# Optimization experiments

Hardware: AMD Instinct MI355X
Metric: run time of the kernel (lower is better)

The kernel has to match this reference:

```python
import jax, jax.numpy as jnp
import numpy as np

B, S, D, H = 64, 2048, 512, 512


def setup_inputs() -> dict:
    key = jax.random.key(0)
    ks = jax.random.split(key, 8)
    inp = jax.random.normal(ks[0], (B, D), dtype=jnp.float32)
    context = jax.random.normal(ks[1], (B, S, D), dtype=jnp.float32)
    mask = jax.random.randint(ks[2], (B, S), 0, 2).astype(jnp.int32)
    alpha_mask = jax.random.uniform(ks[3], (B, S), dtype=jnp.float32)
    sd = 1.0 / np.sqrt(D)
    W_in = jax.random.uniform(ks[4], (H, D), minval=-sd, maxval=sd, dtype=jnp.float32)
    b_in = jnp.zeros((H,), dtype=jnp.float32)
    W_ctx = jax.random.uniform(ks[5], (H, D), minval=-sd, maxval=sd, dtype=jnp.float32)  # Conv1d k=1 == pointwise linear
    b_ctx = jnp.zeros((H,), dtype=jnp.float32)
    V = jax.random.uniform(ks[6], (H,), minval=-1.0, maxval=1.0, dtype=jnp.float32)
    return {"input": inp, "context": context, "alpha_mask": alpha_mask,
            "W_in": W_in, "b_in": b_in, "W_ctx": W_ctx, "b_ctx": b_ctx, "V": V,
            "mask": mask}


def reference(input, context, alpha_mask, W_in, b_in, W_ctx, b_ctx, V, mask):
    seq_len = context.shape[1]
    # input_linear: [B, H]
    inp = input @ W_in.T + b_in
    # context_linear (Conv1d kernel=1 over permuted context): [B, H, S]
    ctx = jnp.einsum('hd,bsd->bhs', W_ctx, context) + b_ctx[None, :, None]
    # additive attention energies: V . tanh(inp + ctx) -> [B, S]
    att = jnp.einsum('h,bhs->bs', V, jnp.tanh(inp[:, :, None] + ctx))
    # mask branching (faithful to the torch data-dependent branch, jit-safe):
    # if any(mask) and count(mask) == S: att[mask] = -inf; else: att = att * alpha_mask
    mb = mask != 0
    n_true = jnp.sum(mb)
    take_inf_branch = (n_true > 0) & (n_true == seq_len)
    att = jnp.where(take_inf_branch,
                    jnp.where(mb, -jnp.inf, att),
                    att * alpha_mask)
    alpha = jax.nn.softmax(att, axis=-1)  # [B, S]
    # context vector: bmm(ctx [B,H,S], alpha [B,S,1]) -> [B, H]
    hidden_state = jnp.einsum('bhs,bs->bh', ctx, alpha)
    return hidden_state, alpha
```

## Files before the change

kernel.cpp:

```cpp
#include <hip/hip_runtime.h>
#include <math.h>

#define B 64
#define S 2048
#define D 512
#define H 512

#define BK 64
#define WSC 128

typedef _Float16 f16x8 __attribute__((ext_vector_type(8)));
typedef __fp16 fp16x2 __attribute__((ext_vector_type(2)));
typedef float f32x4 __attribute__((ext_vector_type(4)));

#define WS_PART_OFF (512 * 1024)
#define WS_CNT_OFF  (512 * 1024 + 2 * 1024 * 1024)

__global__ __launch_bounds__(256) void k_pack_wc(
        const float* __restrict__ Wc, _Float16* __restrict__ wsB,
        int* __restrict__ cnt) {
    if (blockIdx.x == 0 && threadIdx.x == 0) *cnt = 0;
    const int slot = blockIdx.x * 256 + threadIdx.x;
    const int st   = slot >> 11;
    const int rem  = slot & 2047;
    const int hg   = rem >> 6;
    const int lane = rem & 63;
    const int h  = hg * 16 + (lane & 15);
    const int k0 = st * 32 + (lane >> 4) * 8;
    const float* src = Wc + (size_t)h * D + k0;
    float4 f0 = *(const float4*)src;
    float4 f1 = *(const float4*)(src + 4);
    f16x8 v;
    v[0] = (_Float16)f0.x; v[1] = (_Float16)f0.y;
    v[2] = (_Float16)f0.z; v[3] = (_Float16)f0.w;
    v[4] = (_Float16)f1.x; v[5] = (_Float16)f1.y;
    v[6] = (_Float16)f1.z; v[7] = (_Float16)f1.w;
    *(f16x8*)(wsB + (size_t)slot * 8) = v;
}

__global__ __launch_bounds__(256) void k_mask_count(
        const int* __restrict__ mask, int* __restrict__ cnt) {
    const int base = blockIdx.x * 256 + threadIdx.x;
    int local = 0;
    for (int i = base; i < B * S; i += 256 * 64) local += (mask[i] != 0) ? 1 : 0;
    #pragma unroll
    for (int off = 32; off; off >>= 1) local += __shfl_down(local, off, 64);
    if ((threadIdx.x & 63) == 0 && local) atomicAdd(cnt, local);
}

__global__ __launch_bounds__(256) void k_input_linear(
        const float* __restrict__ input,
        const float* __restrict__ W_in,
        const float* __restrict__ b_in,
        float* __restrict__ out_inp) {
    const int b = blockIdx.x;
    const int tid = threadIdx.x;
    __shared__ float xrow[D];
    for (int d = tid; d < D; d += 256) xrow[d] = input[(size_t)b * D + d];
    __syncthreads();
    for (int h = tid; h < H; h += 256) {
        const float* w = W_in + (size_t)h * D;
        float acc = 0.f;
        #pragma unroll 4
        for (int d = 0; d < D; d += 4) {
            float4 wv = *(const float4*)(w + d);
            acc += wv.x * xrow[d] + wv.y * xrow[d + 1] + wv.z * xrow[d + 2] + wv.w * xrow[d + 3];
        }
        out_inp[(size_t)b * H + h] = acc + b_in[h];
    }
}

__global__ __launch_bounds__(512, 4) void k_energy(
        const float* __restrict__ ctx,
        const _Float16* __restrict__ WcP,
        const float* __restrict__ bc,
        const float* __restrict__ inp,
        const float* __restrict__ V,
        float* __restrict__ att) {
    __shared__ alignas(16) _Float16 Alds[2][64 * BK];
    __shared__ float red[8][64];

    const int tid = threadIdx.x;
    const int b  = blockIdx.x >> 5;
    const int s0 = (blockIdx.x & 31) << 6;

    const int arow = tid >> 3;
    const int akq  = tid & 7;
    const int wslot = akq ^ (arow & 7);
    const int lane = tid & 63;
    const int w    = tid >> 6;
    const int lrow = lane & 15;
    const int kblk = lane >> 4;

    f32x4 acc[4][4] = {};

    const float* ctx_src = ctx + ((size_t)b * S + s0 + arow) * D + akq * 8;
    const _Float16* Bbase = WcP + ((size_t)(w * 4) * 64 + lane) * 8;
    const int rsw = lrow & 7;

    {
        float4 f0 = *(const float4*)ctx_src;
        float4 f1 = *(const float4*)(ctx_src + 4);
        union { fp16x2 h2[4]; f16x8 v; } u;
        u.h2[0] = __builtin_amdgcn_cvt_pkrtz(f0.x, f0.y);
        u.h2[1] = __builtin_amdgcn_cvt_pkrtz(f0.z, f0.w);
        u.h2[2] = __builtin_amdgcn_cvt_pkrtz(f1.x, f1.y);
        u.h2[3] = __builtin_amdgcn_cvt_pkrtz(f1.z, f1.w);
        *(f16x8*)&Alds[0][arow * BK + wslot * 8] = u.v;
    }
    __syncthreads();

    #pragma unroll 1
    for (int kt = 0; kt < 8; ++kt) {
        const int cur = kt & 1;
        const _Float16* Ab = &Alds[cur][0];
        const size_t st0 = (size_t)(kt * 2) * 2048;
        const size_t st1 = (size_t)(kt * 2 + 1) * 2048;

        f16x8 b00 = *(const f16x8*)(Bbase + (st0 + 0 * 64) * 8);
        f16x8 b01 = *(const f16x8*)(Bbase + (st0 + 1 * 64) * 8);
        f16x8 b02 = *(const f16x8*)(Bbase + (st0 + 2 * 64) * 8);
        f16x8 b03 = *(const f16x8*)(Bbase + (st0 + 3 * 64) * 8);
        __builtin_amdgcn_sched_barrier(0);

        const int sl0 = kblk ^ rsw;
        f16x8 a00 = *(const f16x8*)(Ab + (0 * 16 + lrow) * BK + sl0 * 8);
        f16x8 a01 = *(const f16x8*)(Ab + (1 * 16 + lrow) * BK + sl0 * 8);
        f16x8 a02 = *(const f16x8*)(Ab + (2 * 16 + lrow) * BK + sl0 * 8);
        f16x8 a03 = *(const f16x8*)(Ab + (3 * 16 + lrow) * BK + sl0 * 8);

        f16x8 b10 = *(const f16x8*)(Bbase + (st1 + 0 * 64) * 8);
        f16x8 b11 = *(const f16x8*)(Bbase + (st1 + 1 * 64) * 8);
        f16x8 b12 = *(const f16x8*)(Bbase + (st1 + 2 * 64) * 8);
        f16x8 b13 = *(const f16x8*)(Bbase + (st1 + 3 * 64) * 8);

        {
            f16x8 af_[4] = {a00, a01, a02, a03};
            f16x8 bf_[4] = {b00, b01, b02, b03};
            #pragma unroll
            for (int m = 0; m < 4; ++m)
                #pragma unroll
                for (int n = 0; n < 4; ++n)
                    acc[m][n] = __builtin_amdgcn_mfma_f32_16x16x32_f16(
                        af_[m], bf_[n], acc[m][n], 0, 0, 0);
        }

        float4 nf0, nf1;
        if (kt < 7) {
            nf0 = *(const float4*)(ctx_src + (kt + 1) * BK);
            nf1 = *(const float4*)(ctx_src + (kt + 1) * BK + 4);
        }

        const int sl1 = (4 + kblk) ^ rsw;
        f16x8 a10 = *(const f16x8*)(Ab + (0 * 16 + lrow) * BK + sl1 * 8);
        f16x8 a11 = *(const f16x8*)(Ab + (1 * 16 + lrow) * BK + sl1 * 8);
        f16x8 a12 = *(const f16x8*)(Ab + (2 * 16 + lrow) * BK + sl1 * 8);
        f16x8 a13 = *(const f16x8*)(Ab + (3 * 16 + lrow) * BK + sl1 * 8);
        __builtin_amdgcn_sched_barrier(0);

        {
            f16x8 af_[4] = {a10, a11, a12, a13};
            f16x8 bf_[4] = {b10, b11, b12, b13};
            #pragma unroll
            for (int m = 0; m < 4; ++m)
                #pragma unroll
                for (int n = 0; n < 4; ++n)
                    acc[m][n] = __builtin_amdgcn_mfma_f32_16x16x32_f16(
                        af_[m], bf_[n], acc[m][n], 0, 0, 0);
        }
        __builtin_amdgcn_sched_barrier(0);

        if (kt < 7) {
            union { fp16x2 h2[4]; f16x8 v; } u;
            u.h2[0] = __builtin_amdgcn_cvt_pkrtz(nf0.x, nf0.y);
            u.h2[1] = __builtin_amdgcn_cvt_pkrtz(nf0.z, nf0.w);
            u.h2[2] = __builtin_amdgcn_cvt_pkrtz(nf1.x, nf1.y);
            u.h2[3] = __builtin_amdgcn_cvt_pkrtz(nf1.z, nf1.w);
            *(f16x8*)&Alds[cur ^ 1][arow * BK + wslot * 8] = u.v;
        }
        __syncthreads();
    }

    float ps_[4][4] = {};
    #pragma unroll
    for (int n = 0; n < 4; ++n) {
        const int h = w * 64 + n * 16 + lrow;
        const float ib = inp[(size_t)b * H + h] + bc[h];
        const float v = V[h];
        #pragma unroll
        for (int m = 0; m < 4; ++m)
            #pragma unroll
            for (int r = 0; r < 4; ++r) {
                const float x = acc[m][n][r] + ib;
                const float t = 1.f - 2.f / (1.f + __expf(2.f * x));
                ps_[m][r] += v * t;
            }
    }
    #pragma unroll
    for (int off = 1; off < 16; off <<= 1)
        #pragma unroll
        for (int m = 0; m < 4; ++m)
            #pragma unroll
            for (int r = 0; r < 4; ++r)
                ps_[m][r] += __shfl_xor(ps_[m][r], off, 64);
    if (lrow == 0) {
        #pragma unroll
        for (int m = 0; m < 4; ++m)
            #pragma unroll
            for (int r = 0; r < 4; ++r)
                red[w][m * 16 + kblk * 4 + r] = ps_[m][r];
    }
    __syncthreads();
    if (tid < 64) {
        float sum = 0.f;
        #pragma unroll
        for (int i = 0; i < 8; ++i) sum += red[i][tid];
        att[(size_t)b * S + s0 + tid] = sum;
    }
}

__global__ __launch_bounds__(256) void k_softmax(
        const int* __restrict__ mask,
        const float* __restrict__ amask,
        const int* __restrict__ cnt,
        float* __restrict__ att) {
    const int b = blockIdx.x;
    const int tid = threadIdx.x;
    __shared__ float sh[S];
    __shared__ float fredm[4];
    __shared__ float freds[4];

    const int n_true = *cnt;
    const bool inf_branch = (n_true > 0) && (n_true == S);

    const float NEG_INF = -__builtin_inff();
    for (int s = tid; s < S; s += 256) {
        const float raw = att[(size_t)b * S + s];
        float v;
        if (inf_branch)
            v = mask[(size_t)b * S + s] ? NEG_INF : raw;
        else
            v = raw * amask[(size_t)b * S + s];
        sh[s] = v;
    }
    __syncthreads();

    float mx = NEG_INF;
    for (int s = tid; s < S; s += 256) mx = fmaxf(mx, sh[s]);
    #pragma unroll
    for (int off = 32; off; off >>= 1) mx = fmaxf(mx, __shfl_down(mx, off, 64));
    if ((tid & 63) == 0) fredm[tid >> 6] = mx;
    __syncthreads();
    mx = fmaxf(fmaxf(fredm[0], fredm[1]), fmaxf(fredm[2], fredm[3]));

    float lsum = 0.f;
    for (int s = tid; s < S; s += 256) {
        const float e = expf(sh[s] - mx);
        sh[s] = e;
        lsum += e;
    }
    #pragma unroll
    for (int off = 32; off; off >>= 1) lsum += __shfl_down(lsum, off, 64);
    if ((tid & 63) == 0) freds[tid >> 6] = lsum;
    __syncthreads();
    const float total = freds[0] + freds[1] + freds[2] + freds[3];
    const float rinv = 1.f / total;

    for (int s = tid; s < S; s += 256)
        att[(size_t)b * S + s] = sh[s] * rinv;
}

__global__ __launch_bounds__(256) void k_wsum(
        const float* __restrict__ ctx,
        const float* __restrict__ alpha,
        float* __restrict__ part) {
    const int chunk = blockIdx.x & 15;
    const int b = blockIdx.x >> 4;
    const int s0 = chunk * WSC;
    const int tid = threadIdx.x;
    __shared__ float al[WSC];
    if (tid < WSC) al[tid] = alpha[(size_t)b * S + s0 + tid];
    __syncthreads();

    const int half = tid >> 7;
    const int dq = (tid & 127) * 4;
    const float* base = ctx + ((size_t)b * S + s0 + half) * D + dq;
    float4 acc = {0.f, 0.f, 0.f, 0.f};
    #pragma unroll 4
    for (int i = 0; i < WSC / 2; ++i) {
        float4 v = *(const float4*)(base + (size_t)i * 2 * D);
        const float a = al[i * 2 + half];
        acc.x += a * v.x; acc.y += a * v.y; acc.z += a * v.z; acc.w += a * v.w;
    }
    __shared__ float cb[2][D];
    *(float4*)&cb[half][dq] = acc;
    __syncthreads();
    if (tid < 128) {
        const int d = tid * 4;
        float4 p0 = *(const float4*)&cb[0][d];
        float4 p1 = *(const float4*)&cb[1][d];
        float4 o = {p0.x + p1.x, p0.y + p1.y, p0.z + p1.z, p0.w + p1.w};
        *(float4*)(part + ((size_t)chunk * B + b) * D + d) = o;
    }
}

__global__ __launch_bounds__(256) void k_out(
        const float* __restrict__ part,
        const float* __restrict__ Wc,
        const float* __restrict__ bc,
        float* __restrict__ hidden) {
    const int b = blockIdx.x;
    const int tid = threadIdx.x;
    __shared__ float cb[D];
    for (int d = tid; d < D; d += 256) {
        float s = 0.f;
        #pragma unroll
        for (int c = 0; c < 16; ++c)
            s += part[((size_t)c * B + b) * D + d];
        cb[d] = s;
    }
    __syncthreads();
    for (int h = tid; h < H; h += 256) {
        const float* w = Wc + (size_t)h * D;
        float acc = 0.f;
        #pragma unroll 4
        for (int d = 0; d < D; d += 4) {
            float4 wv = *(const float4*)(w + d);
            acc += wv.x * cb[d] + wv.y * cb[d + 1] + wv.z * cb[d + 2] + wv.w * cb[d + 3];
        }
        hidden[(size_t)b * H + h] = acc + bc[h];
    }
}

extern "C" void kernel_launch(void* const* d_in, const int* in_sizes, int n_in,
                              void* d_out, int out_size, void* d_ws, size_t ws_size,
                              hipStream_t stream) {
    const float* input = (const float*)d_in[0];
    const float* ctx   = (const float*)d_in[1];
    const float* amask = (const float*)d_in[2];
    const float* W_in  = (const float*)d_in[3];
    const float* b_in  = (const float*)d_in[4];
    const float* W_ctx = (const float*)d_in[5];
    const float* b_ctx = (const float*)d_in[6];
    const float* V     = (const float*)d_in[7];
    const int*   mask  = (const int*)d_in[8];

    float* out = (float*)d_out;
    float* hidden = out;
    float* alpha  = out + B * H;

    _Float16* wsB  = (_Float16*)d_ws;
    float*    part = (float*)((char*)d_ws + WS_PART_OFF);
    int*      cnt  = (int*)((char*)d_ws + WS_CNT_OFF);

    k_pack_wc<<<dim3(128), dim3(256), 0, stream>>>(W_ctx, wsB, cnt);
    k_mask_count<<<dim3(64), dim3(256), 0, stream>>>(mask, cnt);

    k_input_linear<<<dim3(B), dim3(256), 0, stream>>>(input, W_in, b_in, hidden);

    k_energy<<<dim3(B * S / 64), dim3(512), 0, stream>>>(
        ctx, wsB, b_ctx, hidden, V, alpha);

    k_softmax<<<dim3(B), dim3(256), 0, stream>>>(mask, amask, cnt, alpha);

    k_wsum<<<dim3(16 * B), dim3(256), 0, stream>>>(ctx, alpha, part);

    k_out<<<dim3(B), dim3(256), 0, stream>>>(part, W_ctx, b_ctx, hidden);
}
```

Before: 231.8 us.

## Cache fp16 context copy in energy kernel for wsum; merge prep kernels

The energy kernel now writes its fp16-converted, swizzled context tiles to a workspace buffer. The weighted-sum kernel reads that half-size copy instead of re-reading the fp32 context, which cuts its main memory traffic. The three small prep kernels (weight pack, input linear, mask count) are merged into one launch, and the mask count uses per-block partial sums instead of an atomic. The cost is extra writes of the fp16 context copy in the energy kernel, a larger workspace, and reduced precision in the weighted sum.

After: 228.6 us, median of 2. About the same (-1.4%).

```diff
diff --git a/kernel.cpp b/kernel.cpp
--- a/kernel.cpp
+++ b/kernel.cpp
@@ -7,66 +7,67 @@
 #define H 512
 
 #define BK 64
-#define WSC 128
 
 typedef _Float16 f16x8 __attribute__((ext_vector_type(8)));
 typedef __fp16 fp16x2 __attribute__((ext_vector_type(2)));
 typedef float f32x4 __attribute__((ext_vector_type(4)));
 
-#define WS_PART_OFF (512 * 1024)
-#define WS_CNT_OFF  (512 * 1024 + 2 * 1024 * 1024)
-
-__global__ __launch_bounds__(256) void k_pack_wc(
+#define WS_PART_OFF  (512 * 1024)
+#define WS_CNT_OFF   (512 * 1024 + 4 * 1024 * 1024)
+#define WS_CTX16_OFF (8 * 1024 * 1024)
+
+__global__ __launch_bounds__(256) void k_prep(
         const float* __restrict__ Wc, _Float16* __restrict__ wsB,
-        int* __restrict__ cnt) {
-    if (blockIdx.x == 0 && threadIdx.x == 0) *cnt = 0;
-    const int slot = blockIdx.x * 256 + threadIdx.x;
-    const int st   = slot >> 11;
-    const int rem  = slot & 2047;
-    const int hg   = rem >> 6;
-    const int lane = rem & 63;
-    const int h  = hg * 16 + (lane & 15);
-    const int k0 = st * 32 + (lane >> 4) * 8;
-    const float* src = Wc + (size_t)h * D + k0;
-    float4 f0 = *(const float4*)src;
-    float4 f1 = *(const float4*)(src + 4);
-    f16x8 v;
-    v[0] = (_Float16)f0.x; v[1] = (_Float16)f0.y;
-    v[2] = (_Float16)f0.z; v[3] = (_Float16)f0.w;
-    v[4] = (_Float16)f1.x; v[5] = (_Float16)f1.y;
-    v[6] = (_Float16)f1.z; v[7] = (_Float16)f1.w;
-    *(f16x8*)(wsB + (size_t)slot * 8) = v;
-}
-
-__global__ __launch_bounds__(256) void k_mask_count(
-        const int* __restrict__ mask, int* __restrict__ cnt) {
-    const int base = blockIdx.x * 256 + threadIdx.x;
-    int local = 0;
-    for (int i = base; i < B * S; i += 256 * 64) local += (mask[i] != 0) ? 1 : 0;
-    #pragma unroll
-    for (int off = 32; off; off >>= 1) local += __shfl_down(local, off, 64);
-    if ((threadIdx.x & 63) == 0 && local) atomicAdd(cnt, local);
-}
-
-__global__ __launch_bounds__(256) void k_input_linear(
-        const float* __restrict__ input,
-        const float* __restrict__ W_in,
-        const float* __restrict__ b_in,
-        float* __restrict__ out_inp) {
-    const int b = blockIdx.x;
-    const int tid = threadIdx.x;
-    __shared__ float xrow[D];
-    for (int d = tid; d < D; d += 256) xrow[d] = input[(size_t)b * D + d];
-    __syncthreads();
-    for (int h = tid; h < H; h += 256) {
-        const float* w = W_in + (size_t)h * D;
-        float acc = 0.f;
-        #pragma unroll 4
-        for (int d = 0; d < D; d += 4) {
-            float4 wv = *(const float4*)(w + d);
-            acc += wv.x * xrow[d] + wv.y * xrow[d + 1] + wv.z * xrow[d + 2] + wv.w * xrow[d + 3];
-        }
-        out_inp[(size_t)b * H + h] = acc + b_in[h];
+        const float* __restrict__ input, const float* __restrict__ W_in,
+        const float* __restrict__ b_in, float* __restrict__ out_inp,
+        const int* __restrict__ mask, int* __restrict__ cntArr) {
+    const int bid = blockIdx.x;
+    const int tid = threadIdx.x;
+
+    if (bid < 128) {
+        const int slot = bid * 256 + tid;
+        const int st   = slot >> 11;
+        const int rem  = slot & 2047;
+        const int hg   = rem >> 6;
+        const int lane = rem & 63;
+        const int h  = hg * 16 + (lane & 15);
+        const int k0 = st * 32 + (lane >> 4) * 8;
+        const float* src = Wc + (size_t)h * D + k0;
+        float4 f0 = *(const float4*)src;
+        float4 f1 = *(const float4*)(src + 4);
+        f16x8 v;
+        v[0] = (_Float16)f0.x; v[1] = (_Float16)f0.y;
+        v[2] = (_Float16)f0.z; v[3] = (_Float16)f0.w;
+        v[4] = (_Float16)f1.x; v[5] = (_Float16)f1.y;
+        v[6] = (_Float16)f1.z; v[7] = (_Float16)f1.w;
+        *(f16x8*)(wsB + (size_t)slot * 8) = v;
+    } else if (bid < 192) {
+        const int b = bid - 128;
+        __shared__ float xrow[D];
+        for (int d = tid; d < D; d += 256) xrow[d] = input[(size_t)b * D + d];
+        __syncthreads();
+        for (int h = tid; h < H; h += 256) {
+            const float* w = W_in + (size_t)h * D;
+            float acc = 0.f;
+            #pragma unroll 4
+            for (int d = 0; d < D; d += 4) {
+                float4 wv = *(const float4*)(w + d);
+                acc += wv.x * xrow[d] + wv.y * xrow[d + 1] + wv.z * xrow[d + 2] + wv.w * xrow[d + 3];
+            }
+            out_inp[(size_t)b * H + h] = acc + b_in[h];
+        }
+    } else {
+        const int i0 = (bid - 192) * 2048;
+        int local = 0;
+        #pragma unroll
+        for (int it = 0; it < 8; ++it)
+            local += (mask[i0 + it * 256 + tid] != 0) ? 1 : 0;
+        #pragma unroll
+        for (int off = 32; off; off >>= 1) local += __shfl_down(local, off, 64);
+        __shared__ int ired[4];
+        if ((tid & 63) == 0) ired[tid >> 6] = local;
+        __syncthreads();
+        if (tid == 0) cntArr[bid - 192] = ired[0] + ired[1] + ired[2] + ired[3];
     }
 }
 
@@ -76,7 +77,8 @@
         const float* __restrict__ bc,
         const float* __restrict__ inp,
         const float* __restrict__ V,
-        float* __restrict__ att) {
+        float* __restrict__ att,
+        _Float16* __restrict__ ctx16) {
     __shared__ alignas(16) _Float16 Alds[2][64 * BK];
     __shared__ float red[8][64];
 
@@ -87,6 +89,7 @@
     const int arow = tid >> 3;
     const int akq  = tid & 7;
     const int wslot = akq ^ (arow & 7);
+    const int toff = arow * 64 + wslot * 8;
     const int lane = tid & 63;
     const int w    = tid >> 6;
     const int lrow = lane & 15;
@@ -96,6 +99,7 @@
 
     const float* ctx_src = ctx + ((size_t)b * S + s0 + arow) * D + akq * 8;
     const _Float16* Bbase = WcP + ((size_t)(w * 4) * 64 + lane) * 8;
+    _Float16* wb = ctx16 + (size_t)blockIdx.x * 32768;
     const int rsw = lrow & 7;
 
     {
@@ -106,7 +110,8 @@
         u.h2[1] = __builtin_amdgcn_cvt_pkrtz(f0.z, f0.w);
         u.h2[2] = __builtin_amdgcn_cvt_pkrtz(f1.x, f1.y);
         u.h2[3] = __builtin_amdgcn_cvt_pkrtz(f1.z, f1.w);
-        *(f16x8*)&Alds[0][arow * BK + wslot * 8] = u.v;
+        *(f16x8*)&Alds[0][toff] = u.v;
+        *(f16x8*)(wb + toff) = u.v;
     }
     __syncthreads();
 
@@ -176,7 +181,8 @@
             u.h2[1] = __builtin_amdgcn_cvt_pkrtz(nf0.z, nf0.w);
             u.h2[2] = __builtin_amdgcn_cvt_pkrtz(nf1.x, nf1.y);
             u.h2[3] = __builtin_amdgcn_cvt_pkrtz(nf1.z, nf1.w);
-            *(f16x8*)&Alds[cur ^ 1][arow * BK + wslot * 8] = u.v;
+            *(f16x8*)&Alds[cur ^ 1][toff] = u.v;
+            *(f16x8*)(wb + (size_t)(kt + 1) * 4096 + toff) = u.v;
         }
         __syncthreads();
     }
@@ -222,7 +228,7 @@
 __global__ __launch_bounds__(256) void k_softmax(
         const int* __restrict__ mask,
         const float* __restrict__ amask,
-        const int* __restrict__ cnt,
+        const int* __restrict__ cntArr,
         float* __restrict__ att) {
     const int b = blockIdx.x;
     const int tid = threadIdx.x;
@@ -230,7 +236,9 @@
     __shared__ float fredm[4];
     __shared__ float freds[4];
 
-    const int n_true = *cnt;
+    int n_true = 0;
+    #pragma unroll
+    for (int i = 0; i < 64; ++i) n_true += cntArr[i];
     const bool inf_branch = (n_true > 0) && (n_true == S);
 
     const float NEG_INF = -__builtin_inff();
@@ -271,36 +279,46 @@
 }
 
 __global__ __launch_bounds__(256) void k_wsum(
-        const float* __restrict__ ctx,
+        const _Float16* __restrict__ ctx16,
         const float* __restrict__ alpha,
         float* __restrict__ part) {
-    const int chunk = blockIdx.x & 15;
-    const int b = blockIdx.x >> 4;
-    const int s0 = chunk * WSC;
-    const int tid = threadIdx.x;
-    __shared__ float al[WSC];
-    if (tid < WSC) al[tid] = alpha[(size_t)b * S + s0 + tid];
-    __syncthreads();
-
-    const int half = tid >> 7;
-    const int dq = (tid & 127) * 4;
-    const float* base = ctx + ((size_t)b * S + s0 + half) * D + dq;
-    float4 acc = {0.f, 0.f, 0.f, 0.f};
+    const int eb = blockIdx.x;
+    const int b = eb >> 5;
+    const int c = eb & 31;
+    const int s0 = c * 64;
+    const int tid = threadIdx.x;
+    const int ko = tid & 63;
+    const int rg = tid >> 6;
+
+    __shared__ float al[64];
+    if (tid < 64) al[tid] = alpha[(size_t)b * S + s0 + tid];
+    __syncthreads();
+
+    const _Float16* base = ctx16 + (size_t)eb * 32768 + (size_t)(ko >> 3) * 4096;
+    const int q = ko & 7;
+
+    float acc[8] = {};
     #pragma unroll 4
-    for (int i = 0; i < WSC / 2; ++i) {
-        float4 v = *(const float4*)(base + (size_t)i * 2 * D);
-        const float a = al[i * 2 + half];
-        acc.x += a * v.x; acc.y += a * v.y; acc.z += a * v.z; acc.w += a * v.w;
-    }
-    __shared__ float cb[2][D];
-    *(float4*)&cb[half][dq] = acc;
+    for (int rr = 0; rr < 16; ++rr) {
+        const int r = rg * 16 + rr;
+        f16x8 v = *(const f16x8*)(base + r * 64 + (q ^ (r & 7)) * 8);
+        const float a = al[r];
+        #pragma unroll
+        for (int j = 0; j < 8; ++j) acc[j] += a * (float)v[j];
+    }
+
+    __shared__ float red[4][512];
+    #pragma unroll
+    for (int j = 0; j < 8; ++j) red[rg][ko * 8 + j] = acc[j];
     __syncthreads();
     if (tid < 128) {
         const int d = tid * 4;
-        float4 p0 = *(const float4*)&cb[0][d];
-        float4 p1 = *(const float4*)&cb[1][d];
-        float4 o = {p0.x + p1.x, p0.y + p1.y, p0.z + p1.z, p0.w + p1.w};
-        *(float4*)(part + ((size_t)chunk * B + b) * D + d) = o;
+        float4 o;
+        o.x = red[0][d + 0] + red[1][d + 0] + red[2][d + 0] + red[3][d + 0];
+        o.y = red[0][d + 1] + red[1][d + 1] + red[2][d + 1] + red[3][d + 1];
+        o.z = red[0][d + 2] + red[1][d + 2] + red[2][d + 2] + red[3][d + 2];
+        o.w = red[0][d + 3] + red[1][d + 3] + red[2][d + 3] + red[3][d + 3];
+        *(float4*)(part + ((size_t)c * B + b) * D + d) = o;
     }
 }
 
@@ -315,7 +333,7 @@
     for (int d = tid; d < D; d += 256) {
         float s = 0.f;
         #pragma unroll
-        for (int c = 0; c < 16; ++c)
+        for (int c = 0; c < 32; ++c)
             s += part[((size_t)c * B + b) * D + d];
         cb[d] = s;
     }
@@ -349,21 +367,20 @@
     float* hidden = out;
     float* alpha  = out + B * H;
 
-    _Float16* wsB  = (_Float16*)d_ws;
-    float*    part = (float*)((char*)d_ws + WS_PART_OFF);
-    int*      cnt  = (int*)((char*)d_ws + WS_CNT_OFF);
-
-    k_pack_wc<<<dim3(128), dim3(256), 0, stream>>>(W_ctx, wsB, cnt);
-    k_mask_count<<<dim3(64), dim3(256), 0, stream>>>(mask, cnt);
-
-    k_input_linear<<<dim3(B), dim3(256), 0, stream>>>(input, W_in, b_in, hidden);
+    _Float16* wsB    = (_Float16*)d_ws;
+    float*    part   = (float*)((char*)d_ws + WS_PART_OFF);
+    int*      cntArr = (int*)((char*)d_ws + WS_CNT_OFF);
+    _Float16* ctx16  = (_Float16*)((char*)d_ws + WS_CTX16_OFF);
+
+    k_prep<<<dim3(256), dim3(256), 0, stream>>>(
+        W_ctx, wsB, input, W_in, b_in, hidden, mask, cntArr);
 
     k_energy<<<dim3(B * S / 64), dim3(512), 0, stream>>>(
-        ctx, wsB, b_ctx, hidden, V, alpha);
-
-    k_softmax<<<dim3(B), dim3(256), 0, stream>>>(mask, amask, cnt, alpha);
-
-    k_wsum<<<dim3(16 * B), dim3(256), 0, stream>>>(ctx, alpha, part);
+        ctx, wsB, b_ctx, hidden, V, alpha, ctx16);
+
+    k_softmax<<<dim3(B), dim3(256), 0, stream>>>(mask, amask, cntArr, alpha);
+
+    k_wsum<<<dim3(B * 32), dim3(256), 0, stream>>>(ctx16, alpha, part);
 
     k_out<<<dim3(B), dim3(256), 0, stream>>>(part, W_ctx, b_ctx, hidden);
 }
```
